# Kernel tuning notes

Measured on AMD Instinct MI355X. Metric: run time of the kernel, lower is better.

Reference implementation:

```python
import jax, jax.numpy as jnp
import numpy as np

B, C, H, W = 8, 512, 32, 32
N = H * W
FG_THRES, BG_THRES, TOPK = 0.7, 0.6, 12


def setup_inputs() -> dict:
    key = jax.random.key(0)
    k1, k2, k3 = jax.random.split(key, 3)
    feature_q = jax.random.normal(k1, (B, C, H, W), dtype=jnp.float32)
    support_feat = jax.random.normal(k2, (B, C, H, W), dtype=jnp.float32)
    support_mask = jax.random.randint(k3, (B, H, W), 0, 2).astype(jnp.int32)
    return {"feature_q": feature_q, "support_feat": support_feat, "support_mask": support_mask}


def _masked_avg_pool(feat, mask):
    # feat [B,C,H,W], mask [B,1,H,W]; interpolate to same size is identity
    return jnp.sum(feat * mask, axis=(2, 3)) / (jnp.sum(mask, axis=(2, 3)) + 1e-5)


def _cosine(a, b):
    # F.cosine_similarity along channel dim 1 (eps=1e-8), with broadcasting
    dot = jnp.sum(a * b, axis=1)
    na = jnp.sqrt(jnp.sum(a * a, axis=1))
    nb = jnp.sqrt(jnp.sum(b * b, axis=1))
    return dot / jnp.maximum(na * nb, 1e-8)


def _similarity(feature_q, fg_proto, bg_proto):
    sim_fg = _cosine(feature_q, fg_proto)
    sim_bg = _cosine(feature_q, bg_proto)
    return jnp.stack([sim_bg, sim_fg], axis=1) * 10.0  # [B,2,H,W]


def _select_weights(pred, thres):
    # pred [N] -> float {0,1} selection weights; threshold mask, topk-12 fallback
    m = pred > thres
    _, top_idx = jax.lax.top_k(pred, TOPK)
    tm = jnp.zeros_like(m).at[top_idx].set(True)
    return jnp.where(m.sum() > 0, m, tm).astype(pred.dtype)


def _ssp_single(cur_feat, pred_fg, pred_bg):
    # cur_feat [C,N]; masked formulation == torch's variable-length column select
    wf = _select_weights(pred_fg, FG_THRES)
    wb = _select_weights(pred_bg, BG_THRES)
    fg_proto = jnp.sum(cur_feat * wf, axis=-1) / wf.sum()  # [C]
    bg_proto = jnp.sum(cur_feat * wb, axis=-1) / wb.sum()
    cn = cur_feat / jnp.sqrt(jnp.sum(cur_feat * cur_feat, axis=0, keepdims=True))
    sim = (cn.T @ cn) * 2.0  # [N,N] cosine sim, scaled
    neg = jnp.asarray(-1e30, sim.dtype)
    fg_attn = jax.nn.softmax(jnp.where(wf[None, :] > 0, sim, neg), axis=-1)
    bg_attn = jax.nn.softmax(jnp.where(wb[None, :] > 0, sim, neg), axis=-1)
    fg_local = (fg_attn @ cur_feat.T).T  # [C,N]
    bg_local = (bg_attn @ cur_feat.T).T
    return fg_proto, bg_proto, fg_local, bg_local


def reference(feature_q, support_feat, support_mask):
    mask_f = (support_mask == 1).astype(feature_q.dtype)[:, None]  # [B,1,H,W]
    mask_b = (support_mask == 0).astype(feature_q.dtype)[:, None]
    FP = _masked_avg_pool(support_feat, mask_f)[:, :, None, None]  # [B,C,1,1]
    BP = _masked_avg_pool(support_feat, mask_b)[:, :, None, None]
    out_0 = _similarity(feature_q, FP, BP)  # [B,2,H,W]
    pred = jax.nn.softmax(out_0, axis=1).reshape(B, 2, N)
    cur = feature_q.reshape(B, C, N)
    fg_p, bg_p, fg_l, bg_l = jax.vmap(_ssp_single)(cur, pred[:, 1], pred[:, 0])
    SSFP = fg_p[:, :, None, None]
    SSBP = bg_p[:, :, None, None]
    ASBP = bg_l.reshape(B, C, H, W)
    FP_1 = FP * 0.5 + SSFP * 0.5
    BP_1 = SSBP * 0.3 + ASBP * 0.7
    out_1 = _similarity(feature_q, FP_1, BP_1)  # [B,2,H,W]
    return out_1
```

## Files before the change

kernel.cpp:

```cpp
#include <hip/hip_runtime.h>
#include <math.h>

#define Bsz 8
#define Cch 512
#define Npx 1024
#define TOPK 12
#define BN (Bsz * Npx)

typedef __attribute__((ext_vector_type(8))) short bf16x8;
typedef __attribute__((ext_vector_type(4))) float f32x4;

__device__ __forceinline__ unsigned short f2bf(float x) {
    unsigned u = __float_as_uint(x);
    u += 0x7FFF + ((u >> 16) & 1);
    return (unsigned short)(u >> 16);
}
__device__ __forceinline__ float bf2f(unsigned short h) {
    return __uint_as_float(((unsigned)h) << 16);
}

__device__ __forceinline__ float warp_sum64(float v) {
    for (int o = 32; o > 0; o >>= 1) v += __shfl_down(v, o);
    return v;
}
__device__ __forceinline__ float block_sum512(float v, float* s8) {
    v = warp_sum64(v);
    int lane = threadIdx.x & 63, w = threadIdx.x >> 6;
    __syncthreads();
    if (lane == 0) s8[w] = v;
    __syncthreads();
    float r = 0.f;
    #pragma unroll
    for (int k = 0; k < 8; k++) r += s8[k];
    return r;
}

__global__ void k_pool(const float* __restrict__ sf, const int* __restrict__ mask,
                       float* __restrict__ FPo, float* __restrict__ BPo) {
    __shared__ float s4a[4], s4b[4], s4c[4];
    int c = blockIdx.x, b = blockIdx.y, t = threadIdx.x;
    const float4* f4 = (const float4*)(sf + ((size_t)b * Cch + c) * Npx);
    const int4* m4 = (const int4*)(mask + (size_t)b * Npx);
    float4 v = f4[t];
    int4 m = m4[t];
    float sumf = (m.x == 1 ? v.x : 0.f) + (m.y == 1 ? v.y : 0.f)
               + (m.z == 1 ? v.z : 0.f) + (m.w == 1 ? v.w : 0.f);
    float tot = v.x + v.y + v.z + v.w;
    float cf = (float)((m.x == 1) + (m.y == 1) + (m.z == 1) + (m.w == 1));
    sumf = warp_sum64(sumf);
    tot  = warp_sum64(tot);
    cf   = warp_sum64(cf);
    int lane = t & 63, w = t >> 6;
    if (lane == 0) { s4a[w] = sumf; s4b[w] = tot; s4c[w] = cf; }
    __syncthreads();
    if (t == 0) {
        float sA = s4a[0] + s4a[1] + s4a[2] + s4a[3];
        float sB = s4b[0] + s4b[1] + s4b[2] + s4b[3];
        float sC = s4c[0] + s4c[1] + s4c[2] + s4c[3];
        FPo[b * Cch + c] = sA / (sC + 1e-5f);
        BPo[b * Cch + c] = (sB - sA) / ((1024.f - sC) + 1e-5f);
    }
}

__global__ void __launch_bounds__(512) k_predcast(const float* __restrict__ fq,
                       const float* __restrict__ FP, const float* __restrict__ BP,
                       float* __restrict__ dsim, float* __restrict__ invn,
                       unsigned short* __restrict__ Ft) {
    __shared__ float sFP[Cch], sBP[Cch], s8[8];
    __shared__ float rdf[16][32], rdb[16][32], rqq[16][32];
    __shared__ unsigned short S[32][522];
    int b = blockIdx.y, t = threadIdx.x;
    int tx = t & 31, ty = t >> 5;
    int p0 = blockIdx.x * 32;
    int p = p0 + tx;
    sFP[t] = FP[b * Cch + t];
    sBP[t] = BP[b * Cch + t];
    __syncthreads();
    float nf = sqrtf(block_sum512(sFP[t] * sFP[t], s8));
    float nb = sqrtf(block_sum512(sBP[t] * sBP[t], s8));
    const float* q = fq + (size_t)b * Cch * Npx + p;
    float df = 0.f, db = 0.f, qq = 0.f;
    int c0 = ty * 32;
    #pragma unroll 4
    for (int c = 0; c < 32; c += 2) {
        float v0 = q[(size_t)(c0 + c) * Npx];
        float v1 = q[(size_t)(c0 + c + 1) * Npx];
        df += v0 * sFP[c0 + c] + v1 * sFP[c0 + c + 1];
        db += v0 * sBP[c0 + c] + v1 * sBP[c0 + c + 1];
        qq += v0 * v0 + v1 * v1;
        unsigned pk = (unsigned)f2bf(v0) | ((unsigned)f2bf(v1) << 16);
        *(unsigned*)&S[tx][c0 + c] = pk;
    }
    rdf[ty][tx] = df; rdb[ty][tx] = db; rqq[ty][tx] = qq;
    __syncthreads();
    for (int s = 8; s > 0; s >>= 1) {
        if (ty < s) {
            rdf[ty][tx] += rdf[ty + s][tx];
            rdb[ty][tx] += rdb[ty + s][tx];
            rqq[ty][tx] += rqq[ty + s][tx];
        }
        __syncthreads();
    }
    if (ty == 0) {
        float nq = sqrtf(rqq[0][tx]);
        float simf = 10.f * rdf[0][tx] / fmaxf(nq * nf, 1e-8f);
        float simb = 10.f * rdb[0][tx] / fmaxf(nq * nb, 1e-8f);
        dsim[b * Npx + p] = simf - simb;
        invn[b * Npx + p] = 1.f / nq;
    }
    int w = t >> 6, lane = t & 63;
    unsigned short* FtB = Ft + (size_t)b * Npx * Cch;
    for (int pr = w; pr < 32; pr += 8) {
        unsigned* dst = (unsigned*)(FtB + (size_t)(p0 + pr) * Cch);
        #pragma unroll
        for (int it = 0; it < 4; it++) {
            int d = it * 64 + lane;
            dst[d] = *(const unsigned*)&S[pr][d * 2];
        }
    }
}

__global__ void __launch_bounds__(1024) k_selcompact(const float* __restrict__ dsim,
                        const float* __restrict__ invn,
                        const unsigned short* __restrict__ Ft,
                        const float* __restrict__ FP,
                        int* __restrict__ nsf, int* __restrict__ nsb,
                        int* __restrict__ jf, int* __restrict__ jb,
                        float* __restrict__ ivg,
                        float* __restrict__ fgp, float* __restrict__ bgp,
                        float* __restrict__ FP1, float* __restrict__ nfv) {
    __shared__ int wsum[16];
    __shared__ int sns;
    __shared__ float sProto[16][512];
    __shared__ float s16f[16];
    int b = blockIdx.y, t = threadIdx.x;
    int lane = t & 63, w = t >> 6;
    bool isf = (blockIdx.x == 0);
    float d = dsim[b * Npx + t];
    float key = isf ? d : -d;
    float thres = isf ? 0.8472979f : 0.4054651f;
    int flag = (key > thres) ? 1 : 0;
    int x = flag;
    #pragma unroll
    for (int o = 1; o < 64; o <<= 1) {
        int y = __shfl_up(x, o);
        if (lane >= o) x += y;
    }
    if (lane == 63) wsum[w] = x;
    __syncthreads();
    int base = 0, total = 0;
    #pragma unroll
    for (int k = 0; k < 16; k++) {
        int s = wsum[k];
        if (k < w) base += s;
        total += s;
    }
    int* jdst = (isf ? jf : jb) + b * Npx;
    if (total == 0) {
        __shared__ int   sc[Npx];
        __shared__ float v[Npx];
        __shared__ float rv[Npx];
        __shared__ int   ri[Npx];
        v[t] = key; flag = 0;
        __syncthreads();
        for (int k = 0; k < TOPK; k++) {
            rv[t] = v[t]; ri[t] = t;
            __syncthreads();
            for (int s = 512; s > 0; s >>= 1) {
                if (t < s) {
                    float a = rv[t], bb = rv[t + s];
                    int ia = ri[t], ib = ri[t + s];
                    if (bb > a || (bb == a && ib < ia)) { rv[t] = bb; ri[t] = ib; }
                }
                __syncthreads();
            }
            int win = ri[0];
            if (t == win) { flag = 1; v[t] = -INFINITY; }
            __syncthreads();
        }
        sc[t] = flag;
        __syncthreads();
        for (int off = 1; off < 1024; off <<= 1) {
            int xx = (t >= off) ? sc[t - off] : 0;
            __syncthreads();
            sc[t] += xx;
            __syncthreads();
        }
        if (flag) {
            int pos = sc[t] - 1;
            jdst[pos] = t;
            if (!isf) ivg[b * Npx + pos] = invn[b * Npx + t];
        }
        if (t == 1023) sns = sc[1023];
    } else {
        if (flag) {
            int pos = base + x - 1;
            jdst[pos] = t;
            if (!isf) ivg[b * Npx + pos] = invn[b * Npx + t];
        }
        if (t == 0) sns = total;
    }
    __syncthreads();
    int ns = sns;
    if (t == 0) (isf ? nsf : nsb)[b] = ns;
    const unsigned short* FtB = Ft + (size_t)b * Npx * Cch;
    float facc[8] = {0.f, 0.f, 0.f, 0.f, 0.f, 0.f, 0.f, 0.f};
    int k = w;
    int row = (k < ns) ? jdst[k] : 0;
    while (k < ns) {
        int kn = k + 16;
        int rown = (kn < ns) ? jdst[kn] : 0;
        bf16x8 vv = *(const bf16x8*)&FtB[(size_t)row * Cch + lane * 8];
        #pragma unroll
        for (int e = 0; e < 8; e++) facc[e] += bf2f((unsigned short)vv[e]);
        k = kn; row = rown;
    }
    #pragma unroll
    for (int e = 0; e < 8; e++) sProto[w][lane * 8 + e] = facc[e];
    __syncthreads();
    float fp1 = 0.f;
    if (t < 512) {
        float s = 0.f;
        #pragma unroll
        for (int q = 0; q < 16; q++) s += sProto[q][t];
        float pv = s / (float)ns;
        (isf ? fgp : bgp)[b * Cch + t] = pv;
        if (isf) {
            fp1 = 0.5f * FP[b * Cch + t] + 0.5f * pv;
            FP1[b * Cch + t] = fp1;
        }
    }
    if (isf) {
        float v2 = warp_sum64(fp1 * fp1);
        if (lane == 0) s16f[w] = v2;
        __syncthreads();
        if (t == 0) {
            float nn = 0.f;
            #pragma unroll
            for (int q = 0; q < 16; q++) nn += s16f[q];
            nfv[b] = sqrtf(nn);
        }
    }
}

__global__ void __launch_bounds__(512) k_fused(
        const unsigned short* __restrict__ Ft,
        const int* __restrict__ jb, const int* __restrict__ nsb,
        const float* __restrict__ invn, const float* __restrict__ ivg,
        const float* __restrict__ bgp, const float* __restrict__ FP1,
        const float* __restrict__ nfv, float* __restrict__ out) {
    __shared__ unsigned short Afull[32][520];
    __shared__ unsigned short sP[32][1032];
    __shared__ unsigned short Bt[64][136];
    __shared__ int   sji[1024];
    __shared__ float sfj[1024];
    __shared__ float sfi[32], sden[32];
    __shared__ float sfp1c[64], sbgc[64];
    __shared__ float spart[32][4];

    int b = blockIdx.y;
    int i0 = blockIdx.x * 32;
    int tid = threadIdx.x;
    int l = tid & 63, w = tid >> 6;
    int ml = l & 15, quad = l >> 4;
    int ns = nsb[b];
    int K64 = ((((ns + 31) & ~31) + 63) & ~63);

    const unsigned short* FtB = Ft + (size_t)b * Npx * Cch;

    #pragma unroll
    for (int s = 0; s < 4; s++) {
        int idx = tid + s * 512;
        int row = idx >> 6, kc8 = (idx & 63) * 8;
        *(uint4*)&Afull[row][kc8] = *(const uint4*)(FtB + (size_t)(i0 + row) * Cch + kc8);
    }
    for (int j = tid; j < K64; j += 512) {
        sji[j] = (j < ns) ? jb[b * Npx + j] : jb[b * Npx];
        sfj[j] = (j < ns) ? ivg[b * Npx + j] : 0.f;
    }
    if (tid < 32) sfi[tid] = 2.f * invn[b * Npx + i0 + tid];
    __syncthreads();

    int ig = w & 1, jg = w >> 1;
    for (int j0 = 0; j0 < K64; j0 += 64) {
        const unsigned short* pb0 = FtB + (size_t)sji[j0 + (tid >> 4)] * Cch + (tid & 15) * 8;
        const unsigned short* pb1 = FtB + (size_t)sji[j0 + 32 + (tid >> 4)] * Cch + (tid & 15) * 8;
        uint4 v0 = *(const uint4*)pb0;
        uint4 v1 = *(const uint4*)pb1;
        f32x4 acc = {};
        for (int k0 = 0; k0 < Cch; k0 += 128) {
            __syncthreads();
            *(uint4*)&Bt[tid >> 4][(tid & 15) * 8] = v0;
            *(uint4*)&Bt[32 + (tid >> 4)][(tid & 15) * 8] = v1;
            __syncthreads();
            int kn = k0 + 128;
            if (kn < Cch) {
                v0 = *(const uint4*)(pb0 + kn);
                v1 = *(const uint4*)(pb1 + kn);
            }
            #pragma unroll
            for (int h = 0; h < 4; h++) {
                bf16x8 af = *(const bf16x8*)&Afull[ig * 16 + ml][k0 + h * 32 + quad * 8];
                bf16x8 bf = *(const bf16x8*)&Bt[jg * 16 + ml][h * 32 + quad * 8];
                acc = __builtin_amdgcn_mfma_f32_16x16x32_bf16(af, bf, acc, 0, 0, 0);
            }
        }
        #pragma unroll
        for (int r = 0; r < 4; r++) {
            int il = ig * 16 + quad * 4 + r;
            int jl = jg * 16 + ml;
            float e = (j0 + jl < ns) ? __expf(acc[r] * sfi[il] * sfj[j0 + jl]) : 0.f;
            sP[il][j0 + jl] = f2bf(e);
        }
    }
    __syncthreads();

    {
        int i = tid >> 4, jj16 = tid & 15;
        float s = 0.f;
        for (int j = jj16; j < K64; j += 16) s += bf2f(sP[i][j]);
        #pragma unroll
        for (int m = 1; m < 16; m <<= 1) s += __shfl_xor(s, m);
        if (jj16 == 0) sden[i] = s;
    }
    if (tid < 128) ((float*)spart)[tid] = 0.f;
    __syncthreads();

    int cgw = w & 3, igw = w >> 2;
    int icol = igw * 16 + ml;
    float rdi = 1.f / sden[icol];
    float sdb = 0.f, snb = 0.f, sdf = 0.f, sqq = 0.f;
    int jj = tid & 63, cg = tid >> 6;
    for (int c0 = 0; c0 < Cch; c0 += 64) {
        __syncthreads();
        if (tid < 64) {
            sfp1c[tid] = FP1[b * Cch + c0 + tid];
            sbgc[tid]  = 0.3f * bgp[b * Cch + c0 + tid];
        }
        f32x4 accp = {};
        uint4 vv = *(const uint4*)(FtB + (size_t)sji[jj] * Cch + c0 + cg * 8);
        for (int j0 = 0; j0 < K64; j0 += 64) {
            __syncthreads();
            {
                unsigned short* qd = &Bt[cg * 8][jj];
                qd[0]       = (unsigned short)vv.x;  qd[136]     = (unsigned short)(vv.x >> 16);
                qd[2 * 136] = (unsigned short)vv.y;  qd[3 * 136] = (unsigned short)(vv.y >> 16);
                qd[4 * 136] = (unsigned short)vv.z;  qd[5 * 136] = (unsigned short)(vv.z >> 16);
                qd[6 * 136] = (unsigned short)vv.w;  qd[7 * 136] = (unsigned short)(vv.w >> 16);
            }
            __syncthreads();
            int jn = j0 + 64;
            if (jn < K64) vv = *(const uint4*)(FtB + (size_t)sji[jn + jj] * Cch + c0 + cg * 8);
            #pragma unroll
            for (int hh = 0; hh < 2; hh++) {
                bf16x8 af  = *(const bf16x8*)&Bt[cgw * 16 + ml][hh * 32 + quad * 8];
                bf16x8 bfr = *(const bf16x8*)&sP[icol][j0 + hh * 32 + quad * 8];
                accp = __builtin_amdgcn_mfma_f32_16x16x32_bf16(af, bfr, accp, 0, 0, 0);
            }
        }
        #pragma unroll
        for (int r = 0; r < 4; r++) {
            int cl = cgw * 16 + quad * 4 + r;
            float loc = accp[r] * rdi;
            float bp1 = sbgc[cl] + 0.7f * loc;
            float qv = bf2f(Afull[icol][c0 + cl]);
            sdb += qv * bp1;
            snb += bp1 * bp1;
            sdf += qv * sfp1c[cl];
            sqq += qv * qv;
        }
    }
    sdb += __shfl_xor(sdb, 16);  sdb += __shfl_xor(sdb, 32);
    snb += __shfl_xor(snb, 16);  snb += __shfl_xor(snb, 32);
    sdf += __shfl_xor(sdf, 16);  sdf += __shfl_xor(sdf, 32);
    sqq += __shfl_xor(sqq, 16);  sqq += __shfl_xor(sqq, 32);
    if (quad == 0) {
        atomicAdd(&spart[icol][0], sdb);
        atomicAdd(&spart[icol][1], snb);
        atomicAdd(&spart[icol][2], sdf);
        atomicAdd(&spart[icol][3], sqq);
    }
    __syncthreads();
    if (tid < 32) {
        float db = spart[tid][0], nb = spart[tid][1];
        float df = spart[tid][2], qq = spart[tid][3];
        float nq = sqrtf(qq);
        float sb2 = 10.f * db / fmaxf(nq * sqrtf(nb), 1e-8f);
        float sf2 = 10.f * df / fmaxf(nq * nfv[b], 1e-8f);
        out[((size_t)b * 2) * Npx + i0 + tid] = sb2;
        out[((size_t)b * 2 + 1) * Npx + i0 + tid] = sf2;
    }
}

extern "C" void kernel_launch(void* const* d_in, const int* in_sizes, int n_in,
                              void* d_out, int out_size, void* d_ws, size_t ws_size,
                              hipStream_t stream) {
    const float* fq = (const float*)d_in[0];
    const float* sf = (const float*)d_in[1];
    const int* mask = (const int*)d_in[2];
    float* out = (float*)d_out;

    float* ws = (float*)d_ws;
    float* FP    = ws;
    float* BP    = FP + Bsz * Cch;
    float* fgp   = BP + Bsz * Cch;
    float* bgp   = fgp + Bsz * Cch;
    float* FP1   = bgp + Bsz * Cch;
    float* nfv   = FP1 + Bsz * Cch;
    float* dsim  = nfv + 8;
    float* invn  = dsim + BN;
    float* ivg   = invn + BN;
    int*   nsf   = (int*)(ivg + BN);
    int*   nsb   = nsf + 8;
    int*   jf    = nsb + 8;
    int*   jb    = jf + BN;
    unsigned short* Ft = (unsigned short*)(jb + BN);

    k_pool<<<dim3(Cch, Bsz), 256, 0, stream>>>(sf, mask, FP, BP);
    k_predcast<<<dim3(Npx / 32, Bsz), 512, 0, stream>>>(fq, FP, BP, dsim, invn, Ft);
    k_selcompact<<<dim3(2, Bsz), 1024, 0, stream>>>(dsim, invn, Ft, FP, nsf, nsb, jf, jb, ivg, fgp, bgp, FP1, nfv);
    k_fused<<<dim3(32, Bsz), 512, 0, stream>>>(Ft, jb, nsb, invn, ivg, bgp, FP1, nfv, out);
}
```

Baseline: 130.6 us.

## Replace gathered background columns with dense masked attention over all pixels

The fused attention kernel no longer gathers the compacted background-selected columns through an index list. Instead it runs dense contiguous tiles over all 1024 pixels and zeroes unselected columns using a per-pixel weight array (zero when unselected). Tiles grow to 128 columns in the similarity stage and 256 in the aggregation stage. This drops the indirect gather loads and the dependence on the selection count, at the cost of computing the full N×N product even when few columns are selected.

```diff
diff --git a/kernel.cpp b/kernel.cpp
--- a/kernel.cpp
+++ b/kernel.cpp
@@ -126,7 +126,7 @@
                         const float* __restrict__ FP,
                         int* __restrict__ nsf, int* __restrict__ nsb,
                         int* __restrict__ jf, int* __restrict__ jb,
-                        float* __restrict__ ivg,
+                        float* __restrict__ wiv,
                         float* __restrict__ fgp, float* __restrict__ bgp,
                         float* __restrict__ FP1, float* __restrict__ nfv) {
     __shared__ int wsum[16];
@@ -186,20 +186,13 @@
             sc[t] += xx;
             __syncthreads();
         }
-        if (flag) {
-            int pos = sc[t] - 1;
-            jdst[pos] = t;
-            if (!isf) ivg[b * Npx + pos] = invn[b * Npx + t];
-        }
+        if (flag) jdst[sc[t] - 1] = t;
         if (t == 1023) sns = sc[1023];
     } else {
-        if (flag) {
-            int pos = base + x - 1;
-            jdst[pos] = t;
-            if (!isf) ivg[b * Npx + pos] = invn[b * Npx + t];
-        }
+        if (flag) jdst[base + x - 1] = t;
         if (t == 0) sns = total;
     }
+    if (!isf) wiv[b * Npx + t] = flag ? invn[b * Npx + t] : 0.f;
     __syncthreads();
     int ns = sns;
     if (t == 0) (isf ? nsf : nsb)[b] = ns;
@@ -245,15 +238,13 @@
 
 __global__ void __launch_bounds__(512) k_fused(
         const unsigned short* __restrict__ Ft,
-        const int* __restrict__ jb, const int* __restrict__ nsb,
-        const float* __restrict__ invn, const float* __restrict__ ivg,
+        const float* __restrict__ wiv, const float* __restrict__ invn,
         const float* __restrict__ bgp, const float* __restrict__ FP1,
         const float* __restrict__ nfv, float* __restrict__ out) {
     __shared__ unsigned short Afull[32][520];
     __shared__ unsigned short sP[32][1032];
-    __shared__ unsigned short Bt[64][136];
-    __shared__ int   sji[1024];
-    __shared__ float sfj[1024];
+    __shared__ unsigned short Buf[128 * 136];
+    __shared__ float sWiv[Npx];
     __shared__ float sfi[32], sden[32];
     __shared__ float sfp1c[64], sbgc[64];
     __shared__ float spart[32][4];
@@ -263,9 +254,6 @@
     int tid = threadIdx.x;
     int l = tid & 63, w = tid >> 6;
     int ml = l & 15, quad = l >> 4;
-    int ns = nsb[b];
-    int K64 = ((((ns + 31) & ~31) + 63) & ~63);
-
     const unsigned short* FtB = Ft + (size_t)b * Npx * Cch;
 
     #pragma unroll
@@ -274,43 +262,47 @@
         int row = idx >> 6, kc8 = (idx & 63) * 8;
         *(uint4*)&Afull[row][kc8] = *(const uint4*)(FtB + (size_t)(i0 + row) * Cch + kc8);
     }
-    for (int j = tid; j < K64; j += 512) {
-        sji[j] = (j < ns) ? jb[b * Npx + j] : jb[b * Npx];
-        sfj[j] = (j < ns) ? ivg[b * Npx + j] : 0.f;
-    }
+    #pragma unroll
+    for (int s = 0; s < 2; s++) sWiv[tid + s * 512] = wiv[b * Npx + tid + s * 512];
     if (tid < 32) sfi[tid] = 2.f * invn[b * Npx + i0 + tid];
-    __syncthreads();
 
     int ig = w & 1, jg = w >> 1;
-    for (int j0 = 0; j0 < K64; j0 += 64) {
-        const unsigned short* pb0 = FtB + (size_t)sji[j0 + (tid >> 4)] * Cch + (tid & 15) * 8;
-        const unsigned short* pb1 = FtB + (size_t)sji[j0 + 32 + (tid >> 4)] * Cch + (tid & 15) * 8;
-        uint4 v0 = *(const uint4*)pb0;
-        uint4 v1 = *(const uint4*)pb1;
-        f32x4 acc = {};
+    int brow = tid >> 2, bk = (tid & 3) * 32;
+    for (int j0 = 0; j0 < Npx; j0 += 128) {
+        const unsigned short* src = FtB + (size_t)(j0 + brow) * Cch + bk;
+        uint4 v0 = *(const uint4*)src;
+        uint4 v1 = *(const uint4*)(src + 8);
+        uint4 v2 = *(const uint4*)(src + 16);
+        uint4 v3 = *(const uint4*)(src + 24);
+        f32x4 acc0 = {}, acc1 = {};
         for (int k0 = 0; k0 < Cch; k0 += 128) {
             __syncthreads();
-            *(uint4*)&Bt[tid >> 4][(tid & 15) * 8] = v0;
-            *(uint4*)&Bt[32 + (tid >> 4)][(tid & 15) * 8] = v1;
+            unsigned short* bd = &Buf[brow * 136 + bk];
+            *(uint4*)bd = v0;        *(uint4*)(bd + 8) = v1;
+            *(uint4*)(bd + 16) = v2; *(uint4*)(bd + 24) = v3;
             __syncthreads();
             int kn = k0 + 128;
             if (kn < Cch) {
-                v0 = *(const uint4*)(pb0 + kn);
-                v1 = *(const uint4*)(pb1 + kn);
+                v0 = *(const uint4*)(src + kn);      v1 = *(const uint4*)(src + kn + 8);
+                v2 = *(const uint4*)(src + kn + 16); v3 = *(const uint4*)(src + kn + 24);
             }
             #pragma unroll
             for (int h = 0; h < 4; h++) {
                 bf16x8 af = *(const bf16x8*)&Afull[ig * 16 + ml][k0 + h * 32 + quad * 8];
-                bf16x8 bf = *(const bf16x8*)&Bt[jg * 16 + ml][h * 32 + quad * 8];
-                acc = __builtin_amdgcn_mfma_f32_16x16x32_bf16(af, bf, acc, 0, 0, 0);
+                bf16x8 bf0 = *(const bf16x8*)&Buf[(jg * 32 + ml) * 136 + h * 32 + quad * 8];
+                bf16x8 bf1 = *(const bf16x8*)&Buf[(jg * 32 + 16 + ml) * 136 + h * 32 + quad * 8];
+                acc0 = __builtin_amdgcn_mfma_f32_16x16x32_bf16(af, bf0, acc0, 0, 0, 0);
+                acc1 = __builtin_amdgcn_mfma_f32_16x16x32_bf16(af, bf1, acc1, 0, 0, 0);
             }
         }
         #pragma unroll
         for (int r = 0; r < 4; r++) {
             int il = ig * 16 + quad * 4 + r;
-            int jl = jg * 16 + ml;
-            float e = (j0 + jl < ns) ? __expf(acc[r] * sfi[il] * sfj[j0 + jl]) : 0.f;
-            sP[il][j0 + jl] = f2bf(e);
+            float fi = sfi[il];
+            int jl0 = j0 + jg * 32 + ml;
+            float w0 = sWiv[jl0], w1 = sWiv[jl0 + 16];
+            sP[il][jl0]      = f2bf(w0 > 0.f ? __expf(acc0[r] * fi * w0) : 0.f);
+            sP[il][jl0 + 16] = f2bf(w1 > 0.f ? __expf(acc1[r] * fi * w1) : 0.f);
         }
     }
     __syncthreads();
@@ -318,7 +310,7 @@
     {
         int i = tid >> 4, jj16 = tid & 15;
         float s = 0.f;
-        for (int j = jj16; j < K64; j += 16) s += bf2f(sP[i][j]);
+        for (int j = jj16; j < Npx; j += 16) s += bf2f(sP[i][j]);
         #pragma unroll
         for (int m = 1; m < 16; m <<= 1) s += __shfl_xor(s, m);
         if (jj16 == 0) sden[i] = s;
@@ -330,7 +322,7 @@
     int icol = igw * 16 + ml;
     float rdi = 1.f / sden[icol];
     float sdb = 0.f, snb = 0.f, sdf = 0.f, sqq = 0.f;
-    int jj = tid & 63, cg = tid >> 6;
+    int jr = tid >> 1, ch0 = (tid & 1) * 32;
     for (int c0 = 0; c0 < Cch; c0 += 64) {
         __syncthreads();
         if (tid < 64) {
@@ -338,23 +330,39 @@
             sbgc[tid]  = 0.3f * bgp[b * Cch + c0 + tid];
         }
         f32x4 accp = {};
-        uint4 vv = *(const uint4*)(FtB + (size_t)sji[jj] * Cch + c0 + cg * 8);
-        for (int j0 = 0; j0 < K64; j0 += 64) {
+        const unsigned short* vsrc = FtB + (size_t)jr * Cch + c0 + ch0;
+        uint4 u0 = *(const uint4*)vsrc;
+        uint4 u1 = *(const uint4*)(vsrc + 8);
+        uint4 u2 = *(const uint4*)(vsrc + 16);
+        uint4 u3 = *(const uint4*)(vsrc + 24);
+        for (int j0 = 0; j0 < Npx; j0 += 256) {
             __syncthreads();
             {
-                unsigned short* qd = &Bt[cg * 8][jj];
-                qd[0]       = (unsigned short)vv.x;  qd[136]     = (unsigned short)(vv.x >> 16);
-                qd[2 * 136] = (unsigned short)vv.y;  qd[3 * 136] = (unsigned short)(vv.y >> 16);
-                qd[4 * 136] = (unsigned short)vv.z;  qd[5 * 136] = (unsigned short)(vv.z >> 16);
-                qd[6 * 136] = (unsigned short)vv.w;  qd[7 * 136] = (unsigned short)(vv.w >> 16);
-            }
-            __syncthreads();
-            int jn = j0 + 64;
-            if (jn < K64) vv = *(const uint4*)(FtB + (size_t)sji[jn + jj] * Cch + c0 + cg * 8);
+                unsigned short* vd = &Buf[ch0 * 264 + jr];
+                unsigned uu[8] = {u0.x, u0.y, u0.z, u0.w, u1.x, u1.y, u1.z, u1.w};
+                #pragma unroll
+                for (int e = 0; e < 8; e++) {
+                    vd[(2 * e) * 264]     = (unsigned short)uu[e];
+                    vd[(2 * e + 1) * 264] = (unsigned short)(uu[e] >> 16);
+                }
+                unsigned ww[8] = {u2.x, u2.y, u2.z, u2.w, u3.x, u3.y, u3.z, u3.w};
+                #pragma unroll
+                for (int e = 0; e < 8; e++) {
+                    vd[(16 + 2 * e) * 264] = (unsigned short)ww[e];
+                    vd[(17 + 2 * e) * 264] = (unsigned short)(ww[e] >> 16);
+                }
+            }
+            __syncthreads();
+            int jn = j0 + 256;
+            if (jn < Npx) {
+                const unsigned short* vs2 = FtB + (size_t)(jn + jr) * Cch + c0 + ch0;
+                u0 = *(const uint4*)vs2;        u1 = *(const uint4*)(vs2 + 8);
+                u2 = *(const uint4*)(vs2 + 16); u3 = *(const uint4*)(vs2 + 24);
+            }
             #pragma unroll
-            for (int hh = 0; hh < 2; hh++) {
-                bf16x8 af  = *(const bf16x8*)&Bt[cgw * 16 + ml][hh * 32 + quad * 8];
-                bf16x8 bfr = *(const bf16x8*)&sP[icol][j0 + hh * 32 + quad * 8];
+            for (int js = 0; js < 256; js += 32) {
+                bf16x8 af  = *(const bf16x8*)&Buf[(cgw * 16 + ml) * 264 + js + quad * 8];
+                bf16x8 bfr = *(const bf16x8*)&sP[icol][j0 + js + quad * 8];
                 accp = __builtin_amdgcn_mfma_f32_16x16x32_bf16(af, bfr, accp, 0, 0, 0);
             }
         }
@@ -409,8 +417,8 @@
     float* nfv   = FP1 + Bsz * Cch;
     float* dsim  = nfv + 8;
     float* invn  = dsim + BN;
-    float* ivg   = invn + BN;
-    int*   nsf   = (int*)(ivg + BN);
+    float* wiv   = invn + BN;
+    int*   nsf   = (int*)(wiv + BN);
     int*   nsb   = nsf + 8;
     int*   jf    = nsb + 8;
     int*   jb    = jf + BN;
@@ -418,6 +426,6 @@
 
     k_pool<<<dim3(Cch, Bsz), 256, 0, stream>>>(sf, mask, FP, BP);
     k_predcast<<<dim3(Npx / 32, Bsz), 512, 0, stream>>>(fq, FP, BP, dsim, invn, Ft);
-    k_selcompact<<<dim3(2, Bsz), 1024, 0, stream>>>(dsim, invn, Ft, FP, nsf, nsb, jf, jb, ivg, fgp, bgp, FP1, nfv);
-    k_fused<<<dim3(32, Bsz), 512, 0, stream>>>(Ft, jb, nsb, invn, ivg, bgp, FP1, nfv, out);
-}
+    k_selcompact<<<dim3(2, Bsz), 1024, 0, stream>>>(dsim, invn, Ft, FP, nsf, nsb, jf, jb, wiv, fgp, bgp, FP1, nfv);
+    k_fused<<<dim3(32, Bsz), 512, 0, stream>>>(Ft, wiv, invn, bgp, FP1, nfv, out);
+}
```

Result: slower. 182.4 us (+39.7%).
